# Kernel optimization log

Measured on AMD Instinct MI355X. Metric: run time of the kernel, lower is better.

Reference implementation:

```python
import jax, jax.numpy as jnp
import numpy as np

B, L, E, H, V, DT, C = 64, 80, 256, 256, 30000, 100, 4
D = 4 * L * H  # BatchNorm / FC feature dim = max_length * hidden * 4
EPS = 1e-5


def setup_inputs() -> dict:
    key = jax.random.key(0)
    ks = jax.random.split(key, 20)
    n = lambda k, shape, s: jax.random.normal(k, shape, jnp.float32) * s
    g = 1.0 / np.sqrt(H)  # pytorch LSTM init scale
    return {
        "arg1": jax.random.randint(ks[0], (B, L), 0, V, dtype=jnp.int32),
        "arg2": jax.random.randint(ks[1], (B, L), 0, V, dtype=jnp.int32),
        "seq_lengths": jnp.full((B,), L, dtype=jnp.int32),
        "transE1": jax.random.normal(ks[2], (L, DT), jnp.float32),
        "transE2": jax.random.normal(ks[3], (L, DT), jnp.float32),
        # learned parameters
        "table": n(ks[4], (V, E), 0.05),                 # embedding (xavier-ish)
        "Wih_f": n(ks[5], (4 * H, E), g),
        "Whh_f": n(ks[6], (4 * H, H), g),
        "bih_f": n(ks[7], (4 * H,), g),
        "bhh_f": n(ks[8], (4 * H,), g),
        "Wih_b": n(ks[9], (4 * H, E), g),
        "Whh_b": n(ks[10], (4 * H, H), g),
        "bih_b": n(ks[11], (4 * H,), g),
        "bhh_b": n(ks[12], (4 * H,), g),
        "R": jax.random.uniform(ks[13], (2 * E, 2 * E), jnp.float32),  # torch.rand init
        "gamma": jnp.ones((D,), jnp.float32),
        "beta": jnp.zeros((D,), jnp.float32),
        "fcW": n(ks[14], (C, D), 0.01),
        "fcb": jnp.zeros((C,), jnp.float32),
    }


def _lstm_dir(x, Wih, Whh, b):
    # x: (B, L, E); pytorch gate order i, f, g, o
    xg = jnp.einsum('ble,ge->blg', x, Wih) + b          # (B, L, 4H)
    xg = jnp.swapaxes(xg, 0, 1)                         # (L, B, 4H)
    h0 = jnp.zeros((x.shape[0], Whh.shape[1]), x.dtype)

    def step(carry, g_t):
        h, c = carry
        gates = g_t + h @ Whh.T
        i, f, gg, o = jnp.split(gates, 4, axis=-1)
        c = jax.nn.sigmoid(f) * c + jax.nn.sigmoid(i) * jnp.tanh(gg)
        h = jax.nn.sigmoid(o) * jnp.tanh(c)
        return (h, c), h

    _, hs = jax.lax.scan(step, (h0, h0), xg)
    return jnp.swapaxes(hs, 0, 1)                       # (B, L, H)


def _bilstm(x, Wih_f, Whh_f, bih_f, bhh_f, Wih_b, Whh_b, bih_b, bhh_b):
    fwd = _lstm_dir(x, Wih_f, Whh_f, bih_f + bhh_f)
    bwd = _lstm_dir(x[:, ::-1], Wih_b, Whh_b, bih_b + bhh_b)[:, ::-1]
    return jnp.concatenate([fwd, bwd], axis=-1)         # (B, L, 2H)


def _forward(arg1, arg2, transE1, transE2, table, Wih_f, Whh_f, bih_f, bhh_f,
             Wih_b, Whh_b, bih_b, bhh_b, R, gamma, beta, fcW, fcb):
    # deal_transE: relation[i,j] = tanh(mean(arg1_word_i - arg2_word_j));
    # identical for every batch element -> block-diagonal kron.
    m1 = transE1.mean(axis=1)                           # (L,)
    m2 = transE2.mean(axis=1)                           # (L,)
    rel = jnp.tanh(m1[:, None] - m2[None, :])           # (L, L)
    kg = jax.lax.stop_gradient(jnp.kron(jnp.eye(B, dtype=rel.dtype), rel))  # (B*L, B*L)

    e1 = table[arg1]                                    # (B, L, E); dropout p=0 -> identity
    e2 = table[arg2]
    o1 = _bilstm(e1, Wih_f, Whh_f, bih_f, bhh_f, Wih_b, Whh_b, bih_b, bhh_b)
    o2 = _bilstm(e2, Wih_f, Whh_f, bih_f, bhh_f, Wih_b, Whh_b, bih_b, bhh_b)

    N = B * L
    t1 = o1.reshape(N, 2 * H)
    t2 = o2.reshape(N, 2 * H)

    last = jnp.tanh((t1 @ R) @ t2.T) + kg               # (N, N)
    sf1 = jax.nn.softmax(last, axis=1).mean(axis=0)[:, None]  # (N, 1)
    sf2 = jax.nn.softmax(last, axis=0).mean(axis=1)[:, None]  # (N, 1)

    out1 = (t1 * sf2).reshape(B, L, 2 * H)
    out2 = (t2 * sf1).reshape(B, L, 2 * H)
    out = jnp.concatenate([out1, out2], axis=1).reshape(B, -1)  # (B, D)

    # BatchNorm1d in training mode (biased variance over batch)
    mu = out.mean(axis=0)
    var = out.var(axis=0)
    xn = (out - mu) / jnp.sqrt(var + EPS) * gamma + beta

    logits = xn @ fcW.T + fcb
    return jax.nn.log_softmax(logits, axis=1)           # (B, C)


def reference(arg1, arg2, seq_lengths, transE1, transE2, table, Wih_f, Whh_f,
              bih_f, bhh_f, Wih_b, Whh_b, bih_b, bhh_b, R, gamma, beta, fcW, fcb):
    del seq_lengths  # only encodes (B, L), which are static here
    return _forward(arg1, arg2, transE1, transE2, table, Wih_f, Whh_f, bih_f,
                    bhh_f, Wih_b, Whh_b, bih_b, bhh_b, R, gamma, beta, fcW, fcb)
```

## Files before the change

kernel.cpp:

```cpp
#include <hip/hip_runtime.h>
#include <cstddef>
#include <cstdint>

typedef unsigned short ushort_t;

constexpr int B_ = 64, L_ = 80, E_ = 256, H_ = 256, C_ = 4, DT_ = 100;
constexpr int N_ = B_ * L_;
constexpr int G4_ = 4 * H_;
constexpr int DH2_ = 2 * H_;
constexpr int DF_ = 4 * L_ * H_;
constexpr float EPS_ = 1e-5f;
constexpr int FB_USH = 8192;

typedef short s8v __attribute__((ext_vector_type(8)));
typedef float f4v __attribute__((ext_vector_type(4)));
typedef ushort_t us8 __attribute__((ext_vector_type(8)));

__device__ inline ushort_t f2bf_rn(float x) {
    uint32_t u = __builtin_bit_cast(uint32_t, x);
    uint32_t r = (u + 0x7fffu + ((u >> 16) & 1u)) >> 16;
    return (ushort_t)r;
}
__device__ inline float bf2f(ushort_t h) {
    uint32_t u = ((uint32_t)h) << 16;
    return __builtin_bit_cast(float, u);
}
__device__ inline float bf2f_lo(uint32_t u) { return __builtin_bit_cast(float, u << 16); }
__device__ inline float bf2f_hi(uint32_t u) { return __builtin_bit_cast(float, u & 0xffff0000u); }
__device__ inline float rcpf(float x) { return __builtin_amdgcn_rcpf(x); }
__device__ inline float sigm(float x) { return rcpf(1.f + __expf(-x)); }
__device__ inline float tanh_fast(float x) {
    float e2 = __expf(2.f * x);
    return 1.f - 2.f * rcpf(1.f + e2);
}

#define MFMA_B16(a, b, c) __builtin_amdgcn_mfma_f32_16x16x32_bf16((a), (b), (c), 0, 0, 0)

__global__ void k_prep(const int* __restrict__ arg1, const int* __restrict__ arg2,
                       const float* __restrict__ table,
                       const float* __restrict__ tE1, const float* __restrict__ tE2,
                       const float* __restrict__ Wih_f, const float* __restrict__ Wih_b,
                       const float* __restrict__ bih_f, const float* __restrict__ bhh_f,
                       const float* __restrict__ bih_b, const float* __restrict__ bhh_b,
                       const float* __restrict__ R,
                       const float* __restrict__ Whh_f, const float* __restrict__ Whh_b,
                       ushort_t* __restrict__ ehi, ushort_t* __restrict__ elo,
                       ushort_t* __restrict__ Wchi, ushort_t* __restrict__ Wclo,
                       float* __restrict__ bcat,
                       ushort_t* __restrict__ Rthi, ushort_t* __restrict__ Rtlo,
                       ushort_t* __restrict__ Bhi, ushort_t* __restrict__ Blo,
                       ushort_t* __restrict__ fragbuf, int* __restrict__ flags,
                       float* __restrict__ rel) {
    __shared__ float m1[80], m2[80];
    int blk = blockIdx.x;
    int tid = threadIdx.x;
    if (blk < 10240) {
        int r = blk;
        int rr = (r >= N_) ? (r - N_) : r;
        int idx = (r >= N_) ? arg2[rr] : arg1[rr];
        float v = table[(size_t)idx * E_ + tid];
        ushort_t h = f2bf_rn(v);
        ehi[(size_t)r * E_ + tid] = h;
        elo[(size_t)r * E_ + tid] = f2bf_rn(v - bf2f(h));
    } else if (blk < 12288) {
        int i = (blk - 10240) * 256 + tid;
        if (i < 2 * G4_ * E_) {
            float v = (i < G4_ * E_) ? Wih_f[i] : Wih_b[i - G4_ * E_];
            ushort_t h = f2bf_rn(v);
            Wchi[i] = h;
            Wclo[i] = f2bf_rn(v - bf2f(h));
        }
        if (i < 2 * G4_)
            bcat[i] = (i < G4_) ? (bih_f[i] + bhh_f[i]) : (bih_b[i - G4_] + bhh_b[i - G4_]);
        if (i < 512 * 512) {
            int m = i >> 9, k = i & 511;
            float v = R[k * 512 + m];
            ushort_t h = f2bf_rn(v);
            Rthi[i] = h;
            Rtlo[i] = f2bf_rn(v - bf2f(h));
        }
    } else if (blk < 14336) {
        int idx = (blk - 12288) * 256 + tid;
        int e = idx & 7;
        int lane = (idx >> 3) & 63;
        int g = (idx >> 9) & 3;
        int kt = (idx >> 11) & 7;
        int w = (idx >> 14) & 15;
        int d = idx >> 18;
        int c = lane & 15, q = lane >> 4;
        int row = g * 256 + w * 16 + c;
        int k = kt * 32 + q * 8 + e;
        const float* W = d ? Whh_b : Whh_f;
        float v = W[row * 256 + k];
        ushort_t hi = f2bf_rn(v);
        Bhi[idx] = hi;
        Blo[idx] = f2bf_rn(v - bf2f(hi));
    } else if (blk < 14400) {
        int i = (blk - 14336) * 256 + tid;
        if (i < 256) flags[i] = 0;
        uint4* p = (uint4*)fragbuf;
        for (int jj = i; jj < 32768; jj += 64 * 256)
            p[jj] = make_uint4(0u, 0u, 0u, 0u);
    } else {
        if (tid < 80) {
            float s = 0.f;
            for (int k = 0; k < DT_; ++k) s += tE1[tid * DT_ + k];
            m1[tid] = s * (1.0f / DT_);
        } else if (tid < 160) {
            int i = tid - 80;
            float s = 0.f;
            for (int k = 0; k < DT_; ++k) s += tE2[i * DT_ + k];
            m2[i] = s * (1.0f / DT_);
        }
        __syncthreads();
        for (int idx = tid; idx < 80 * 80; idx += 256)
            rel[idx] = tanhf(m1[idx / 80] - m2[idx % 80]);
    }
}

__global__ __launch_bounds__(256, 2) void k_lstm9c(
        const float* __restrict__ xg,
        const ushort_t* __restrict__ Bhi, const ushort_t* __restrict__ Blo,
        ushort_t* __restrict__ o1hi, ushort_t* __restrict__ o1lo,
        ushort_t* __restrict__ o2hi, ushort_t* __restrict__ o2lo,
        ushort_t* __restrict__ fragbuf, int* __restrict__ flags) {
    const int bid = blockIdx.x;
    const int s = bid & 15;
    const int cg = (bid >> 4) & 7;
    const int d = bid >> 7;
    const int tid = threadIdx.x;
    const int g = tid >> 6, lane = tid & 63;
    const int c16 = lane & 15, qq = lane >> 4;

    __shared__ __align__(16) ushort_t Abuf[8192];
    __shared__ float pre[4][16][16];

    s8v bh[8], bl[8];
    {
        const s8v* BH = (const s8v*)Bhi;
        const s8v* BL = (const s8v*)Blo;
        int base = (d * 16 + s) * 2048 + g * 64 + lane;
        #pragma unroll
        for (int kt = 0; kt < 8; ++kt) {
            bh[kt] = BH[base + kt * 256];
            bl[kt] = BL[base + kt * 256];
        }
    }

    const int c_loc = tid >> 4, j = tid & 15;
    const int kglob = s * 16 + j;
    const int p_kt = kglob >> 5;
    const int p_q = (kglob & 31) >> 3, p_e = kglob & 7;
    const int p_lane = c_loc | (p_q << 4);
    const int fb_off = (p_kt * 64 + p_lane) * 8 + p_e;
    const int cc = cg * 16 + c_loc;
    const int w = cc >> 6, bb = cc & 63;
    ushort_t* ophi = w ? o2hi : o1hi;
    ushort_t* oplo = w ? o2lo : o1lo;
    float cst = 0.f;

    const int grp = bid >> 4;
    int* gflags = flags + grp * 16;
    const size_t fbbase = (size_t)grp * 2 * FB_USH;

    for (int t = 0; t < L_; ++t) {
        int l = d ? (L_ - 1 - t) : t;

        float xv[4];
        {
            const float* xp = xg + (size_t)(w * N_ + bb * L_ + l) * 2048
                              + d * 1024 + kglob;
            #pragma unroll
            for (int gg = 0; gg < 4; ++gg) xv[gg] = xp[gg * 256];
        }

        if (t > 0) {
            if (tid < 16) {
                while (__hip_atomic_load(&gflags[tid], __ATOMIC_RELAXED,
                                         __HIP_MEMORY_SCOPE_AGENT) < t)
                    __builtin_amdgcn_s_sleep(2);
            }
            __syncthreads();
        }

        {
            const unsigned long long* src = (const unsigned long long*)(fragbuf
                + fbbase + (size_t)(t & 1) * FB_USH);
            unsigned long long* dst = (unsigned long long*)Abuf;
            #pragma unroll
            for (int r = 0; r < 8; ++r)
                dst[r * 256 + tid] = __hip_atomic_load(
                    &src[r * 256 + tid], __ATOMIC_RELAXED,
                    __HIP_MEMORY_SCOPE_AGENT);
        }
        __syncthreads();

        f4v acc = {0.f, 0.f, 0.f, 0.f};
        {
            const s8v* AH = (const s8v*)&Abuf[0];
            const s8v* AL = (const s8v*)&Abuf[4096];
            #pragma unroll
            for (int kt = 0; kt < 8; ++kt) {
                s8v ah = AH[kt * 64 + lane];
                s8v al = AL[kt * 64 + lane];
                acc = MFMA_B16(ah, bh[kt], acc);
                acc = MFMA_B16(ah, bl[kt], acc);
                acc = MFMA_B16(al, bh[kt], acc);
            }
        }
        #pragma unroll
        for (int r = 0; r < 4; ++r)
            pre[g][qq * 4 + r][c16] = acc[r];
        __syncthreads();

        ushort_t hh, hl;
        size_t oidx;
        {
            float pi = pre[0][c_loc][j] + xv[0];
            float pf = pre[1][c_loc][j] + xv[1];
            float pg = pre[2][c_loc][j] + xv[2];
            float po = pre[3][c_loc][j] + xv[3];
            float si = sigm(pi), sf_ = sigm(pf), so = sigm(po);
            cst = sf_ * cst + si * tanh_fast(pg);
            float h = so * tanh_fast(cst);
            oidx = (size_t)(bb * L_ + l) * DH2_ + d * H_ + kglob;
            hh = f2bf_rn(h);
            hl = f2bf_rn(h - bf2f(hh));
            ushort_t* fbn = fragbuf + fbbase + (size_t)((t + 1) & 1) * FB_USH;
            __hip_atomic_store(&fbn[fb_off], hh, __ATOMIC_RELAXED,
                               __HIP_MEMORY_SCOPE_AGENT);
            __hip_atomic_store(&fbn[4096 + fb_off], hl, __ATOMIC_RELAXED,
                               __HIP_MEMORY_SCOPE_AGENT);
        }
        __syncthreads();

        if (tid == 0)
            __hip_atomic_store(&flags[bid], t + 1, __ATOMIC_RELAXED,
                               __HIP_MEMORY_SCOPE_AGENT);

        ophi[oidx] = hh;
        oplo[oidx] = hl;
    }
}

__global__ __launch_bounds__(256) void k_gemm_bf(
        const ushort_t* __restrict__ Ahi, const ushort_t* __restrict__ Alo,
        const ushort_t* __restrict__ Bthi, const ushort_t* __restrict__ Btlo,
        const float* __restrict__ bias, float* __restrict__ Cout,
        ushort_t* __restrict__ Couthi, ushort_t* __restrict__ Coutlo,
        int M, int Nn, int K) {
    __shared__ ushort_t smpool[4][4096];
    const int tid = threadIdx.x;
    const int w = tid >> 6, lane = tid & 63;
    const int wr = w >> 1, wc = w & 1;
    const int c16 = lane & 15, q4 = lane >> 4;
    const int nbx = Nn >> 7;
    const int cpx = ((M >> 7) * nbx) >> 3;
    const int fid = blockIdx.x;
    const int swz = (fid & 7) * cpx + (fid >> 3);
    const int bx = swz % nbx, by = swz / nbx;
    const int r0 = by * 128, c0 = bx * 128;

    f4v acc[4][4] = {};
    const ushort_t* planes[4] = {
        Ahi + (size_t)r0 * K, Alo + (size_t)r0 * K,
        Bthi + (size_t)c0 * K, Btlo + (size_t)c0 * K };

    for (int kk = 0; kk < K; kk += 32) {
        #pragma unroll
        for (int p = 0; p < 4; ++p) {
            const ushort_t* src = planes[p] + kk;
            #pragma unroll
            for (int it = 0; it < 2; ++it) {
                int idx = it * 256 + tid;
                int row = idx >> 2, q = idx & 3;
                *(us8*)&smpool[p][(q * 128 + row) * 8] =
                    *(const us8*)&src[(size_t)row * K + q * 8];
            }
        }
        __syncthreads();
        s8v ah[4], al[4], bhv[4], blv[4];
        #pragma unroll
        for (int mi = 0; mi < 4; ++mi) {
            int ar = wr * 64 + mi * 16 + c16;
            ah[mi] = *(const s8v*)&smpool[0][(q4 * 128 + ar) * 8];
            al[mi] = *(const s8v*)&smpool[1][(q4 * 128 + ar) * 8];
        }
        #pragma unroll
        for (int ni = 0; ni < 4; ++ni) {
            int br = wc * 64 + ni * 16 + c16;
            bhv[ni] = *(const s8v*)&smpool[2][(q4 * 128 + br) * 8];
            blv[ni] = *(const s8v*)&smpool[3][(q4 * 128 + br) * 8];
        }
        #pragma unroll
        for (int mi = 0; mi < 4; ++mi)
            #pragma unroll
            for (int ni = 0; ni < 4; ++ni) {
                acc[mi][ni] = MFMA_B16(ah[mi], bhv[ni], acc[mi][ni]);
                acc[mi][ni] = MFMA_B16(ah[mi], blv[ni], acc[mi][ni]);
                acc[mi][ni] = MFMA_B16(al[mi], bhv[ni], acc[mi][ni]);
            }
        __syncthreads();
    }
    #pragma unroll
    for (int mi = 0; mi < 4; ++mi)
        #pragma unroll
        for (int rg = 0; rg < 4; ++rg) {
            int row = r0 + wr * 64 + mi * 16 + q4 * 4 + rg;
            #pragma unroll
            for (int ni = 0; ni < 4; ++ni) {
                int col = c0 + wc * 64 + ni * 16 + c16;
                float v = acc[mi][ni][rg] + (bias ? bias[col] : 0.f);
                size_t idx = (size_t)row * Nn + col;
                if (Couthi) {
                    ushort_t h = f2bf_rn(v);
                    Couthi[idx] = h;
                    Coutlo[idx] = f2bf_rn(v - bf2f(h));
                } else {
                    Cout[idx] = v;
                }
            }
        }
}

__global__ __launch_bounds__(256) void k_bigm(
        const ushort_t* __restrict__ uhi, const ushort_t* __restrict__ ulo,
        const ushort_t* __restrict__ vhi, const ushort_t* __restrict__ vlo,
        const float* __restrict__ rel, ushort_t* __restrict__ Ebf,
        float* __restrict__ rowpart, float* __restrict__ colpart) {
    __shared__ ushort_t smpool[4][4096];
    const int tid = threadIdx.x;
    const int w = tid >> 6, lane = tid & 63;
    const int wr = w >> 1, wc = w & 1;
    const int c16 = lane & 15, q4 = lane >> 4;
    const int fid = blockIdx.x;
    const int swz = (fid & 7) * 200 + (fid >> 3);
    const int bx = swz % 40, by = swz / 40;
    const int r0 = by * 128, c0 = bx * 128;

    f4v acc[4][4] = {};
    const ushort_t* planes[4] = {
        uhi + (size_t)r0 * DH2_, ulo + (size_t)r0 * DH2_,
        vhi + (size_t)c0 * DH2_, vlo + (size_t)c0 * DH2_ };

    for (int kk = 0; kk < 16; ++kk) {
        #pragma unroll
        for (int p = 0; p < 4; ++p) {
            const ushort_t* src = planes[p] + kk * 32;
            #pragma unroll
            for (int it = 0; it < 2; ++it) {
                int idx = it * 256 + tid;
                int row = idx >> 2, q = idx & 3;
                *(us8*)&smpool[p][(q * 128 + row) * 8] =
                    *(const us8*)&src[(size_t)row * DH2_ + q * 8];
            }
        }
        __syncthreads();
        s8v ah[4], al[4], bhv[4], blv[4];
        #pragma unroll
        for (int mi = 0; mi < 4; ++mi) {
            int ar = wr * 64 + mi * 16 + c16;
            ah[mi] = *(const s8v*)&smpool[0][(q4 * 128 + ar) * 8];
            al[mi] = *(const s8v*)&smpool[1][(q4 * 128 + ar) * 8];
        }
        #pragma unroll
        for (int ni = 0; ni < 4; ++ni) {
            int br = wc * 64 + ni * 16 + c16;
            bhv[ni] = *(const s8v*)&smpool[2][(q4 * 128 + br) * 8];
            blv[ni] = *(const s8v*)&smpool[3][(q4 * 128 + br) * 8];
        }
        #pragma unroll
        for (int mi = 0; mi < 4; ++mi)
            #pragma unroll
            for (int ni = 0; ni < 4; ++ni) {
                acc[mi][ni] = MFMA_B16(ah[mi], bhv[ni], acc[mi][ni]);
                acc[mi][ni] = MFMA_B16(ah[mi], blv[ni], acc[mi][ni]);
                acc[mi][ni] = MFMA_B16(al[mi], bhv[ni], acc[mi][ni]);
            }
        __syncthreads();
    }

    float* rowred = (float*)&smpool[0][0];
    float* colred = rowred + 128 * 32;

    int gcolv[4], bjv[4], ljv[4];
    #pragma unroll
    for (int ni = 0; ni < 4; ++ni) {
        int coll = wc * 64 + ni * 16 + c16;
        gcolv[ni] = c0 + coll;
        bjv[ni] = gcolv[ni] / 80;
        ljv[ni] = gcolv[ni] - bjv[ni] * 80;
    }
    float csumv[4] = {0.f, 0.f, 0.f, 0.f};
    #pragma unroll
    for (int mi = 0; mi < 4; ++mi) {
        #pragma unroll
        for (int rg = 0; rg < 4; ++rg) {
            int rowl = wr * 64 + mi * 16 + q4 * 4 + rg;
            int grow = r0 + rowl;
            int bi = grow / 80, li = grow - bi * 80;
            float rsum = 0.f;
            #pragma unroll
            for (int ni = 0; ni < 4; ++ni) {
                float v = tanhf(acc[mi][ni][rg]);
                if (bi == bjv[ni]) v += rel[li * 80 + ljv[ni]];
                ushort_t eb = f2bf_rn(__expf(v));
                Ebf[(size_t)grow * N_ + gcolv[ni]] = eb;
                float er = bf2f(eb);
                rsum += er;
                csumv[ni] += er;
            }
            rowred[rowl * 32 + wc * 16 + c16] = rsum;
        }
    }
    #pragma unroll
    for (int ni = 0; ni < 4; ++ni) {
        int coll = wc * 64 + ni * 16 + c16;
        colred[coll * 8 + wr * 4 + q4] = csumv[ni];
    }
    __syncthreads();
    if (tid < 128) {
        float ssum = 0.f;
        #pragma unroll
        for (int t = 0; t < 32; ++t) ssum += rowred[tid * 32 + t];
        rowpart[(size_t)bx * N_ + r0 + tid] = ssum;
    } else {
        int c = tid - 128;
        float ssum = 0.f;
        #pragma unroll
        for (int t = 0; t < 8; ++t) ssum += colred[c * 8 + t];
        colpart[(size_t)by * N_ + c0 + c] = ssum;
    }
}

__global__ void k_redsum(const float* __restrict__ rowpart, const float* __restrict__ colpart,
                         float* __restrict__ rowinv, float* __restrict__ colinv) {
    int i = blockIdx.x * blockDim.x + threadIdx.x;
    if (i < N_) {
        float rs = 0.f, cs = 0.f;
        for (int t = 0; t < 40; ++t) {
            rs += rowpart[(size_t)t * N_ + i];
            cs += colpart[(size_t)t * N_ + i];
        }
        rowinv[i] = 1.f / rs;
        colinv[i] = 1.f / cs;
    }
}

__global__ __launch_bounds__(256) void k_sf2b(const ushort_t* __restrict__ Ebf,
                                              const float* __restrict__ colinv,
                                              float* __restrict__ sf2) {
    int i = blockIdx.x;
    const uint32_t* Erow = (const uint32_t*)(Ebf + (size_t)i * N_);
    float p = 0.f;
    #pragma unroll 2
    for (int j2 = threadIdx.x; j2 < N_ / 2; j2 += 256) {
        uint32_t u = Erow[j2];
        p += bf2f_lo(u) * colinv[j2 * 2] + bf2f_hi(u) * colinv[j2 * 2 + 1];
    }
    __shared__ float red[256];
    red[threadIdx.x] = p;
    __syncthreads();
    for (int ss = 128; ss > 0; ss >>= 1) {
        if (threadIdx.x < ss) red[threadIdx.x] += red[threadIdx.x + ss];
        __syncthreads();
    }
    if (threadIdx.x == 0) sf2[i] = red[0] * (1.f / N_);
}

__global__ __launch_bounds__(256) void k_sf1b(const ushort_t* __restrict__ Ebf,
                                              const float* __restrict__ rowinv,
                                              float* __restrict__ sf1part) {
    int cp = blockIdx.x * 256 + threadIdx.x;
    int rc = blockIdx.y;
    int r0 = rc * 320;
    float a0 = 0.f, a1 = 0.f;
    #pragma unroll 4
    for (int ii = 0; ii < 320; ++ii) {
        int row = r0 + ii;
        uint32_t u = *(const uint32_t*)(Ebf + (size_t)row * N_ + cp * 2);
        float rinv = rowinv[row];
        a0 += bf2f_lo(u) * rinv;
        a1 += bf2f_hi(u) * rinv;
    }
    sf1part[(size_t)rc * N_ + cp * 2] = a0;
    sf1part[(size_t)rc * N_ + cp * 2 + 1] = a1;
}

__global__ void k_sf1red(const float* __restrict__ sf1part, float* __restrict__ sf1) {
    int jj = blockIdx.x * blockDim.x + threadIdx.x;
    if (jj < N_) {
        float s = 0.f;
        for (int t = 0; t < 16; ++t) s += sf1part[(size_t)t * N_ + jj];
        sf1[jj] = s * (1.f / N_);
    }
}

__global__ void k_bnstats(const ushort_t* __restrict__ o1hi, const ushort_t* __restrict__ o1lo,
                          const ushort_t* __restrict__ o2hi, const ushort_t* __restrict__ o2lo,
                          const float* __restrict__ sf1, const float* __restrict__ sf2,
                          float* __restrict__ bnmu, float* __restrict__ bnrstd) {
    int f = blockIdx.x * 256 + threadIdx.x;
    int seg = f / (L_ * DH2_);
    int rem = f - seg * (L_ * DH2_);
    int l = rem >> 9, hh = rem & 511;
    const ushort_t* phi = seg ? o2hi : o1hi;
    const ushort_t* plo = seg ? o2lo : o1lo;
    const float* sf = seg ? sf1 : sf2;
    float s = 0.f, s2 = 0.f;
    for (int b = 0; b < B_; ++b) {
        int row = b * L_ + l;
        size_t idx = (size_t)row * DH2_ + hh;
        float x = (bf2f(phi[idx]) + bf2f(plo[idx])) * sf[row];
        s += x;
        s2 += x * x;
    }
    float mu = s * (1.f / B_);
    float v = fmaxf(s2 * (1.f / B_) - mu * mu, 0.f);
    bnmu[f] = mu;
    bnrstd[f] = rsqrtf(v + EPS_);
}

__global__ __launch_bounds__(256) void k_logits1(
        const ushort_t* __restrict__ o1hi, const ushort_t* __restrict__ o1lo,
        const ushort_t* __restrict__ o2hi, const ushort_t* __restrict__ o2lo,
        const float* __restrict__ sf1, const float* __restrict__ sf2,
        const float* __restrict__ bnmu, const float* __restrict__ bnrstd,
        const float* __restrict__ gamma, const float* __restrict__ beta,
        const float* __restrict__ fcW, float* __restrict__ part) {
    int b = blockIdx.x, ch = blockIdx.y;
    int tid = threadIdx.x;
    int f0 = ch * (DF_ / 5);
    float acc[4] = {0.f, 0.f, 0.f, 0.f};
    for (int f = f0 + tid; f < f0 + DF_ / 5; f += 256) {
        int seg = f / (L_ * DH2_);
        int rem = f - seg * (L_ * DH2_);
        int l = rem >> 9, hh = rem & 511;
        int row = b * L_ + l;
        size_t idx = (size_t)row * DH2_ + hh;
        const ushort_t* phi = seg ? o2hi : o1hi;
        const ushort_t* plo = seg ? o2lo : o1lo;
        float val = (bf2f(phi[idx]) + bf2f(plo[idx])) * (seg ? sf1 : sf2)[row];
        float xn = (val - bnmu[f]) * bnrstd[f] * gamma[f] + beta[f];
        #pragma unroll
        for (int c = 0; c < 4; ++c) acc[c] += xn * fcW[(size_t)c * DF_ + f];
    }
    __shared__ float red[4][257];
    #pragma unroll
    for (int c = 0; c < 4; ++c) red[c][tid] = acc[c];
    __syncthreads();
    for (int ss = 128; ss > 0; ss >>= 1) {
        if (tid < ss)
            #pragma unroll
            for (int c = 0; c < 4; ++c) red[c][tid] += red[c][tid + ss];
        __syncthreads();
    }
    if (tid < 4) part[((size_t)b * 5 + ch) * 4 + tid] = red[tid][0];
}

__global__ void k_logits2(const float* __restrict__ part,
                          const float* __restrict__ fcb,
                          float* __restrict__ dout) {
    int b = blockIdx.x;
    if (threadIdx.x == 0) {
        float lg[4], mx = -1e30f;
        #pragma unroll
        for (int c = 0; c < 4; ++c) {
            float v = fcb[c];
            for (int ch = 0; ch < 5; ++ch) v += part[((size_t)b * 5 + ch) * 4 + c];
            lg[c] = v;
            mx = fmaxf(mx, v);
        }
        float se = 0.f;
        #pragma unroll
        for (int c = 0; c < 4; ++c) se += expf(lg[c] - mx);
        float lse = mx + logf(se);
        #pragma unroll
        for (int c = 0; c < 4; ++c) dout[b * 4 + c] = lg[c] - lse;
    }
}

extern "C" void kernel_launch(void* const* d_in, const int* in_sizes, int n_in,
                              void* d_out, int out_size, void* d_ws, size_t ws_size,
                              hipStream_t stream) {
    const int* arg1 = (const int*)d_in[0];
    const int* arg2 = (const int*)d_in[1];
    const float* tE1 = (const float*)d_in[3];
    const float* tE2 = (const float*)d_in[4];
    const float* table = (const float*)d_in[5];
    const float* Wih_f = (const float*)d_in[6];
    const float* Whh_f = (const float*)d_in[7];
    const float* bih_f = (const float*)d_in[8];
    const float* bhh_f = (const float*)d_in[9];
    const float* Wih_b = (const float*)d_in[10];
    const float* Whh_b = (const float*)d_in[11];
    const float* bih_b = (const float*)d_in[12];
    const float* bhh_b = (const float*)d_in[13];
    const float* R = (const float*)d_in[14];
    const float* gamma = (const float*)d_in[15];
    const float* beta = (const float*)d_in[16];
    const float* fcW = (const float*)d_in[17];
    const float* fcb = (const float*)d_in[18];
    float* dout = (float*)d_out;

    float* ws = (float*)d_ws;
    size_t off = 0;
    auto alloc = [&](size_t n) { float* p = ws + off; off += n; return p; };

    constexpr size_t PL = (size_t)N_ * DH2_;

    float* rel = alloc(80 * 80);
    float* eplanes = alloc((size_t)2 * N_ * E_);
    float* Wcplanes = alloc((size_t)2 * G4_ * E_);
    float* bcat = alloc(2 * G4_);
    float* Rtplanes = alloc((size_t)262144);
    float* planesA = alloc(PL);
    float* planesU = alloc(PL);
    float* rowpart = alloc((size_t)40 * N_);
    float* colpart = alloc((size_t)40 * N_);
    float* rowinv = alloc(N_);
    float* colinv = alloc(N_);
    float* sf1part = alloc((size_t)16 * N_);
    float* sf1 = alloc(N_);
    float* sf2 = alloc(N_);
    float* bnmu = alloc(DF_);
    float* bnrstd = alloc(DF_);
    float* lgpart = alloc((size_t)B_ * 5 * 4);
    ushort_t* Bhi = (ushort_t*)alloc(262144);
    ushort_t* Blo = (ushort_t*)alloc(262144);
    ushort_t* fragbuf = (ushort_t*)alloc(131072);
    int* flags = (int*)alloc(256);
    float* xg = alloc((size_t)N_ * N_);
    ushort_t* Ebf = (ushort_t*)xg;

    ushort_t* ehi = (ushort_t*)eplanes;
    ushort_t* elo = ehi + (size_t)2 * N_ * E_;
    ushort_t* Wchi = (ushort_t*)Wcplanes;
    ushort_t* Wclo = Wchi + (size_t)2 * G4_ * E_;
    ushort_t* Rthi = (ushort_t*)Rtplanes;
    ushort_t* Rtlo = Rthi + 512 * 512;
    ushort_t* o1hi = (ushort_t*)planesA;
    ushort_t* o1lo = o1hi + PL;
    ushort_t* uhi = (ushort_t*)planesU;
    ushort_t* ulo = uhi + PL;
    ushort_t* o2hi = ehi;
    ushort_t* o2lo = elo;

    k_prep<<<14401, 256, 0, stream>>>(arg1, arg2, table, tE1, tE2,
                                      Wih_f, Wih_b, bih_f, bhh_f, bih_b, bhh_b,
                                      R, Whh_f, Whh_b,
                                      ehi, elo, Wchi, Wclo, bcat, Rthi, Rtlo,
                                      Bhi, Blo, fragbuf, flags, rel);
    k_gemm_bf<<<1280, 256, 0, stream>>>(
        ehi, elo, Wchi, Wclo, bcat, xg, nullptr, nullptr, 2 * N_, 2048, E_);
    k_lstm9c<<<256, 256, 0, stream>>>(xg, Bhi, Blo,
                                      o1hi, o1lo, o2hi, o2lo, fragbuf, flags);
    k_gemm_bf<<<160, 256, 0, stream>>>(
        o1hi, o1lo, Rthi, Rtlo, nullptr, nullptr, uhi, ulo, N_, 512, 512);
    k_bigm<<<1600, 256, 0, stream>>>(
        uhi, ulo, o2hi, o2lo, rel, Ebf, rowpart, colpart);
    k_redsum<<<(N_ + 255) / 256, 256, 0, stream>>>(rowpart, colpart, rowinv, colinv);
    k_sf2b<<<N_, 256, 0, stream>>>(Ebf, colinv, sf2);
    k_sf1b<<<dim3(10, 16), 256, 0, stream>>>(Ebf, rowinv, sf1part);
    k_sf1red<<<(N_ + 255) / 256, 256, 0, stream>>>(sf1part, sf1);
    k_bnstats<<<DF_ / 256, 256, 0, stream>>>(o1hi, o1lo, o2hi, o2lo, sf1, sf2,
                                             bnmu, bnrstd);
    k_logits1<<<dim3(B_, 5), 256, 0, stream>>>(o1hi, o1lo, o2hi, o2lo, sf1, sf2,
                                               bnmu, bnrstd, gamma, beta, fcW, lgpart);
    k_logits2<<<B_, 64, 0, stream>>>(lgpart, fcb, dout);
}
```

Baseline: 624.6 us.

## Use per-wave completion flags in LSTM recurrence and merge sf kernels

The LSTM recurrence kernel used to end each step with a block-wide barrier before thread 0 published the step flag. Now each wave waits for its own outstanding stores and publishes its own flag, and consumers poll 64 flags per group instead of 16. This shortens the critical path of the cross-block handoff, at the cost of more flag polling traffic and reliance on s_waitcnt for ordering. Separately, the two softmax-mean kernels are merged into one launch so one kernel launch is saved and the two can run concurrently.

```diff
diff --git a/kernel.cpp b/kernel.cpp
--- a/kernel.cpp
+++ b/kernel.cpp
@@ -97,7 +97,7 @@
         Blo[idx] = f2bf_rn(v - bf2f(hi));
     } else if (blk < 14400) {
         int i = (blk - 14336) * 256 + tid;
-        if (i < 256) flags[i] = 0;
+        if (i < 1024) flags[i] = 0;
         uint4* p = (uint4*)fragbuf;
         for (int jj = i; jj < 32768; jj += 64 * 256)
             p[jj] = make_uint4(0u, 0u, 0u, 0u);
@@ -118,7 +118,7 @@
     }
 }
 
-__global__ __launch_bounds__(256, 2) void k_lstm9c(
+__global__ __launch_bounds__(256, 2) void k_lstm9d(
         const float* __restrict__ xg,
         const ushort_t* __restrict__ Bhi, const ushort_t* __restrict__ Blo,
         ushort_t* __restrict__ o1hi, ushort_t* __restrict__ o1lo,
@@ -160,7 +160,7 @@
     float cst = 0.f;
 
     const int grp = bid >> 4;
-    int* gflags = flags + grp * 16;
+    int* gflags = flags + grp * 64;
     const size_t fbbase = (size_t)grp * 2 * FB_USH;
 
     for (int t = 0; t < L_; ++t) {
@@ -175,7 +175,7 @@
         }
 
         if (t > 0) {
-            if (tid < 16) {
+            if (tid < 64) {
                 while (__hip_atomic_load(&gflags[tid], __ATOMIC_RELAXED,
                                          __HIP_MEMORY_SCOPE_AGENT) < t)
                     __builtin_amdgcn_s_sleep(2);
@@ -232,10 +232,10 @@
             __hip_atomic_store(&fbn[4096 + fb_off], hl, __ATOMIC_RELAXED,
                                __HIP_MEMORY_SCOPE_AGENT);
         }
-        __syncthreads();
-
-        if (tid == 0)
-            __hip_atomic_store(&flags[bid], t + 1, __ATOMIC_RELAXED,
+
+        asm volatile("s_waitcnt vmcnt(0)" ::: "memory");
+        if (lane == 0)
+            __hip_atomic_store(&flags[bid * 4 + g], t + 1, __ATOMIC_RELAXED,
                                __HIP_MEMORY_SCOPE_AGENT);
 
         ophi[oidx] = hh;
@@ -447,44 +447,44 @@
     }
 }
 
-__global__ __launch_bounds__(256) void k_sf2b(const ushort_t* __restrict__ Ebf,
-                                              const float* __restrict__ colinv,
-                                              float* __restrict__ sf2) {
-    int i = blockIdx.x;
-    const uint32_t* Erow = (const uint32_t*)(Ebf + (size_t)i * N_);
-    float p = 0.f;
-    #pragma unroll 2
-    for (int j2 = threadIdx.x; j2 < N_ / 2; j2 += 256) {
-        uint32_t u = Erow[j2];
-        p += bf2f_lo(u) * colinv[j2 * 2] + bf2f_hi(u) * colinv[j2 * 2 + 1];
-    }
-    __shared__ float red[256];
-    red[threadIdx.x] = p;
-    __syncthreads();
-    for (int ss = 128; ss > 0; ss >>= 1) {
-        if (threadIdx.x < ss) red[threadIdx.x] += red[threadIdx.x + ss];
-        __syncthreads();
-    }
-    if (threadIdx.x == 0) sf2[i] = red[0] * (1.f / N_);
-}
-
-__global__ __launch_bounds__(256) void k_sf1b(const ushort_t* __restrict__ Ebf,
-                                              const float* __restrict__ rowinv,
-                                              float* __restrict__ sf1part) {
-    int cp = blockIdx.x * 256 + threadIdx.x;
-    int rc = blockIdx.y;
-    int r0 = rc * 320;
-    float a0 = 0.f, a1 = 0.f;
-    #pragma unroll 4
-    for (int ii = 0; ii < 320; ++ii) {
-        int row = r0 + ii;
-        uint32_t u = *(const uint32_t*)(Ebf + (size_t)row * N_ + cp * 2);
-        float rinv = rowinv[row];
-        a0 += bf2f_lo(u) * rinv;
-        a1 += bf2f_hi(u) * rinv;
-    }
-    sf1part[(size_t)rc * N_ + cp * 2] = a0;
-    sf1part[(size_t)rc * N_ + cp * 2 + 1] = a1;
+__global__ __launch_bounds__(256) void k_sfboth(
+        const ushort_t* __restrict__ Ebf,
+        const float* __restrict__ rowinv, const float* __restrict__ colinv,
+        float* __restrict__ sf1part, float* __restrict__ sf2) {
+    if (blockIdx.x < N_) {
+        int i = blockIdx.x;
+        const uint32_t* Erow = (const uint32_t*)(Ebf + (size_t)i * N_);
+        float p = 0.f;
+        #pragma unroll 2
+        for (int j2 = threadIdx.x; j2 < N_ / 2; j2 += 256) {
+            uint32_t u = Erow[j2];
+            p += bf2f_lo(u) * colinv[j2 * 2] + bf2f_hi(u) * colinv[j2 * 2 + 1];
+        }
+        __shared__ float red[256];
+        red[threadIdx.x] = p;
+        __syncthreads();
+        for (int ss = 128; ss > 0; ss >>= 1) {
+            if (threadIdx.x < ss) red[threadIdx.x] += red[threadIdx.x + ss];
+            __syncthreads();
+        }
+        if (threadIdx.x == 0) sf2[i] = red[0] * (1.f / N_);
+    } else {
+        int b2 = blockIdx.x - N_;
+        int cpb = b2 % 10, rc = b2 / 10;
+        int cp = cpb * 256 + threadIdx.x;
+        int r0 = rc * 320;
+        float a0 = 0.f, a1 = 0.f;
+        #pragma unroll 4
+        for (int ii = 0; ii < 320; ++ii) {
+            int row = r0 + ii;
+            uint32_t u = *(const uint32_t*)(Ebf + (size_t)row * N_ + cp * 2);
+            float rinv = rowinv[row];
+            a0 += bf2f_lo(u) * rinv;
+            a1 += bf2f_hi(u) * rinv;
+        }
+        sf1part[(size_t)rc * N_ + cp * 2] = a0;
+        sf1part[(size_t)rc * N_ + cp * 2 + 1] = a1;
+    }
 }
 
 __global__ void k_sf1red(const float* __restrict__ sf1part, float* __restrict__ sf1) {
@@ -629,7 +629,7 @@
     ushort_t* Bhi = (ushort_t*)alloc(262144);
     ushort_t* Blo = (ushort_t*)alloc(262144);
     ushort_t* fragbuf = (ushort_t*)alloc(131072);
-    int* flags = (int*)alloc(256);
+    int* flags = (int*)alloc(1024);
     float* xg = alloc((size_t)N_ * N_);
     ushort_t* Ebf = (ushort_t*)xg;
 
@@ -653,15 +653,14 @@
                                       Bhi, Blo, fragbuf, flags, rel);
     k_gemm_bf<<<1280, 256, 0, stream>>>(
         ehi, elo, Wchi, Wclo, bcat, xg, nullptr, nullptr, 2 * N_, 2048, E_);
-    k_lstm9c<<<256, 256, 0, stream>>>(xg, Bhi, Blo,
+    k_lstm9d<<<256, 256, 0, stream>>>(xg, Bhi, Blo,
                                       o1hi, o1lo, o2hi, o2lo, fragbuf, flags);
     k_gemm_bf<<<160, 256, 0, stream>>>(
         o1hi, o1lo, Rthi, Rtlo, nullptr, nullptr, uhi, ulo, N_, 512, 512);
     k_bigm<<<1600, 256, 0, stream>>>(
         uhi, ulo, o2hi, o2lo, rel, Ebf, rowpart, colpart);
     k_redsum<<<(N_ + 255) / 256, 256, 0, stream>>>(rowpart, colpart, rowinv, colinv);
-    k_sf2b<<<N_, 256, 0, stream>>>(Ebf, colinv, sf2);
-    k_sf1b<<<dim3(10, 16), 256, 0, stream>>>(Ebf, rowinv, sf1part);
+    k_sfboth<<<N_ + 160, 256, 0, stream>>>(Ebf, rowinv, colinv, sf1part, sf2);
     k_sf1red<<<(N_ + 255) / 256, 256, 0, stream>>>(sf1part, sf1);
     k_bnstats<<<DF_ / 256, 256, 0, stream>>>(o1hi, o1lo, o2hi, o2lo, sf1, sf2,
                                              bnmu, bnrstd);
```

After: 704.5 us. 1.13x slower.
